# Optimization experiments

Hardware: AMD Instinct MI355X
Metric: run time of the kernel (lower is better)

## Reference

```python
import jax, jax.numpy as jnp
import numpy as np

IMG = 224
NUM_VIEWS = 6
K = 5  # splat kernel size (5x5 = 25 offsets)


def setup_inputs() -> dict:
    key = jax.random.key(0)
    points = jax.random.normal(key, (16, 32768, 3), dtype=jnp.float32)
    return {"points": points}


def _render(points):
    B, N, _ = points.shape
    deg2rad = jnp.pi / 180.0
    az = jnp.linspace(0.0, 360.0, NUM_VIEWS + 1)[:-1] * deg2rad          # (V,)
    el = jnp.array([0.0, 30.0, -30.0, 0.0, 0.0, 0.0])[:NUM_VIEWS] * deg2rad

    # 5x5 splat offsets in normalized coords, matching torch meshgrid(ij) + stack([dx,dy])
    off = jnp.linspace(-2.0 / IMG, 2.0 / IMG, K)
    dyg, dxg = jnp.meshgrid(off, off, indexing="ij")
    koff = jnp.stack([dxg, dyg], axis=-1).reshape(-1, 2)                  # (25, 2)

    def one_view(a, e):
        x, y, z = points[..., 0], points[..., 1], points[..., 2]
        x_rot = x * jnp.cos(a) - z * jnp.sin(a)
        z_rot = x * jnp.sin(a) + z * jnp.cos(a)
        y_rot = y * jnp.cos(e) - z_rot * jnp.sin(e)
        z_fin = y * jnp.sin(e) + z_rot * jnp.cos(e)                       # (B, N)
        p2d = jnp.stack([x_rot, y_rot], axis=-1)                          # (B, N, 2)

        zmin = jnp.min(z_fin, axis=1, keepdims=True)
        zmax = jnp.max(z_fin, axis=1, keepdims=True)
        feat = 0.3 + 0.7 * (z_fin - zmin) / (zmax - zmin + 1e-6)          # (B, N), in [0.3, 1.0]

        coords = p2d[:, :, None, :] + koff[None, None, :, :]              # (B, N, 25, 2)
        # torch .long() truncates toward zero; astype(int32) does too
        px = ((coords[..., 0] + 1.0) * 0.5 * (IMG - 1)).astype(jnp.int32)
        py = ((coords[..., 1] + 1.0) * 0.5 * (IMG - 1)).astype(jnp.int32)
        valid = (px >= 0) & (px < IMG) & (py >= 0) & (py < IMG)
        # invalid splats routed out-of-bounds and dropped by the scatter
        idx = jnp.where(valid, py * IMG + px, IMG * IMG).reshape(B, -1)   # (B, N*25)
        f = jnp.broadcast_to(feat[:, :, None], (B, N, K * K)).reshape(B, -1)

        def splat(i, fv):
            return jnp.zeros(IMG * IMG, dtype=points.dtype).at[i].max(fv, mode="drop")

        img = jax.vmap(splat)(idx, f).reshape(B, IMG, IMG)
        # all 3 channels receive the identical feature values
        return jnp.broadcast_to(img[:, None], (B, 3, IMG, IMG))

    views = jax.vmap(one_view)(az, el)                                    # (V, B, 3, H, W)
    return jnp.transpose(views, (1, 0, 2, 3, 4))                          # (B, V, 3, H, W)


def reference(points) -> jnp.ndarray:
    return _render(points)
```

## Files before the change

### kernel.cpp

```cpp
#include <hip/hip_runtime.h>
#include <math.h>

#define IMG    224
#define NVIEWS 6
#define BATCH  16
#define NPTS   32768
#define PLANE  (IMG * IMG)
#define HROWS  112
#define TILE_ELEMS (HROWS * IMG)

#define K1_NT    256
#define K1_CHUNK 8
#define K1_NWG   (BATCH * NVIEWS * K1_CHUNK)
#define SEGCAP   1024
#define NSEG     (K1_CHUNK * 4)

#define K2_NT    1024
#define K2_NWG   (BATCH * NVIEWS * 2)

#define WS_MM_OFF   24576
#define WS_BIN_OFF  65536

typedef float fx4 __attribute__((ext_vector_type(4)));

struct ViewTrig {
    float sa[NVIEWS], ca[NVIEWS], se[NVIEWS], ce[NVIEWS];
    float off0, off4;
};

__device__ __forceinline__ float fmul_(float a, float b) {
#pragma clang fp contract(off)
    return a * b;
}
__device__ __forceinline__ float fadd_(float a, float b) {
#pragma clang fp contract(off)
    return a + b;
}
__device__ __forceinline__ float fsub_(float a, float b) {
#pragma clang fp contract(off)
    return a - b;
}
__device__ __forceinline__ int pix_(float c) {
    return (int)fmul_(fadd_(c, 1.0f), 111.5f);
}

__device__ __forceinline__ unsigned fmap_(float f) {
    unsigned b = __float_as_uint(f);
    return b ^ ((unsigned)((int)b >> 31) | 0x80000000u);
}
__device__ __forceinline__ float fmap_inv_(unsigned u) {
    unsigned b = (u & 0x80000000u) ? (u ^ 0x80000000u) : ~u;
    return __uint_as_float(b);
}

__device__ __forceinline__ int lane_prefix_(unsigned long long m) {
    return __builtin_amdgcn_mbcnt_hi((unsigned)(m >> 32),
           __builtin_amdgcn_mbcnt_lo((unsigned)m, 0));
}

__global__ __launch_bounds__(K1_NT, 3) void transform_kernel(
    const float* __restrict__ pts, unsigned* __restrict__ ws, ViewTrig vt)
{
    const int bid   = blockIdx.x;
    const int chunk = bid & (K1_CHUNK - 1);
    const int v     = (bid >> 3) % NVIEWS;
    const int b     = bid / (K1_CHUNK * NVIEWS);
    const int bv    = b * NVIEWS + v;

    const float sa = vt.sa[v], ca = vt.ca[v], se = vt.se[v], ce = vt.ce[v];
    const float off0 = vt.off0, off4 = vt.off4;
    const float4* p4 = (const float4*)(pts + (size_t)b * NPTS * 3);

    const int tid = threadIdx.x, lane = tid & 63, wave = tid >> 6;
    const int segi = chunk * 4 + wave;

    unsigned* counts = ws;
    uint2* minmax = (uint2*)((char*)ws + WS_MM_OFF);
    uint2* bins   = (uint2*)((char*)ws + WS_BIN_OFF);
    uint2* seg0 = bins + ((size_t)((bv * 2 + 0) * NSEG + segi)) * SEGCAP;
    uint2* seg1 = bins + ((size_t)((bv * 2 + 1) * NSEG + segi)) * SEGCAP;

    unsigned q0 = 0, q1 = 0;
    float zmin = INFINITY, zmax = -INFINITY;

    auto do_point = [&](float x, float y, float z) {
        const float zr = fadd_(fmul_(x, sa), fmul_(z, ca));
        const float yr = fsub_(fmul_(y, ce), fmul_(zr, se));
        const float xr = fsub_(fmul_(x, ca), fmul_(z, sa));

        const int x0i = pix_(fadd_(xr, off0));
        const int x1i = pix_(fadd_(xr, off4));
        const int y0i = pix_(fadd_(yr, off0));
        const int y1i = pix_(fadd_(yr, off4));

        const float zf = fmaf(zr, ce, y * se);
        zmin = fminf(zmin, zf);
        zmax = fmaxf(zmax, zf);

        const bool okx = (x1i >= 0) && (x0i <= IMG - 1);
        const bool ok0 = okx && (y1i >= 0)     && (y0i <= HROWS - 1);
        const bool ok1 = okx && (y1i >= HROWS) && (y0i <= IMG - 1);

        const int cx0 = max(x0i, 0);
        const int cx1 = min(x1i, IMG - 1);
        const int cy0 = max(y0i, 0);
        const int cy1 = min(y1i, IMG - 1);
        const unsigned pk = (unsigned)cx0 | ((unsigned)cx1 << 8) |
                            ((unsigned)cy0 << 16) | ((unsigned)cy1 << 24);
        const unsigned fz = fmap_(zf);

        {
            const unsigned long long m = __ballot(ok0);
            if (ok0) seg0[q0 + lane_prefix_(m)] = make_uint2(fz, pk);
            q0 += (unsigned)__popcll(m);
        }
        {
            const unsigned long long m = __ballot(ok1);
            if (ok1) seg1[q1 + lane_prefix_(m)] = make_uint2(fz, pk);
            q1 += (unsigned)__popcll(m);
        }
    };

    #pragma unroll
    for (int kk = 0; kk < 4; ++kk) {
        const int g = chunk * 1024 + kk * K1_NT + tid;
        const float4 A = p4[3 * g + 0];
        const float4 B = p4[3 * g + 1];
        const float4 C = p4[3 * g + 2];
        do_point(A.x, A.y, A.z);
        do_point(A.w, B.x, B.y);
        do_point(B.z, B.w, C.x);
        do_point(C.y, C.z, C.w);
    }

    for (int o = 32; o > 0; o >>= 1) {
        zmin = fminf(zmin, __shfl_down(zmin, o, 64));
        zmax = fmaxf(zmax, __shfl_down(zmax, o, 64));
    }
    if (lane == 0) {
        counts[(bv * 2 + 0) * NSEG + segi] = q0;
        counts[(bv * 2 + 1) * NSEG + segi] = q1;
        minmax[bv * NSEG + segi] = make_uint2(fmap_(zmax), fmap_(-zmin));
    }
}

__global__ __launch_bounds__(K2_NT, 1) void splat_kernel(
    const unsigned* __restrict__ ws, float* __restrict__ out)
{
    extern __shared__ __align__(16) unsigned tile[];
    __shared__ unsigned pref[NSEG + 1];
    __shared__ float sScale, sBias;

    const int bid  = blockIdx.x;
    const int xcd  = bid & 7;
    const int slot = bid >> 3;
    const int hi   = (slot >= 12) ? 1 : 0;
    const int b    = xcd + 8 * hi;
    const int vh   = slot - 12 * hi;
    const int v    = vh >> 1;
    const int h    = vh & 1;
    const int bv   = b * NVIEWS + v;
    const int bvh  = bv * 2 + h;
    const int row0 = h * HROWS;
    const int row1 = row0 + HROWS - 1;

    const int tid = threadIdx.x, lane = tid & 63, wave = tid >> 6;

    const unsigned* counts = ws;
    const uint2* minmax = (const uint2*)((const char*)ws + WS_MM_OFF);
    const uint2* binb   = (const uint2*)((const char*)ws + WS_BIN_OFF)
                        + (size_t)bvh * NSEG * SEGCAP;

    {
        int4* t4 = (int4*)tile;
        for (int i = tid; i < TILE_ELEMS / 4; i += K2_NT)
            t4[i] = make_int4(0, 0, 0, 0);
    }
    if (wave == 0) {
        unsigned c = (lane < NSEG) ? counts[bvh * NSEG + lane] : 0u;
        unsigned inc = c;
        #pragma unroll
        for (int o = 1; o < NSEG; o <<= 1) {
            unsigned t = __shfl_up(inc, o, 64);
            if (lane >= o) inc += t;
        }
        if (lane < NSEG) pref[lane + 1] = inc;
        if (lane == 0)   pref[0] = 0;

        uint2 mm = (lane < NSEG) ? minmax[bv * NSEG + lane] : make_uint2(0u, 0u);
        for (int o = 32; o > 0; o >>= 1) {
            mm.x = max(mm.x, __shfl_down(mm.x, o, 64));
            mm.y = max(mm.y, __shfl_down(mm.y, o, 64));
        }
        if (lane == 0) {
            const float mx = fmap_inv_(mm.x);
            const float mn = -fmap_inv_(mm.y);
            const float scale = 0.7f / ((mx - mn) + 1e-6f);
            sScale = scale;
            sBias  = 0.3f - mn * scale;
        }
    }
    __syncthreads();

    const unsigned n = pref[NSEG];
    for (unsigned e = tid; e < n; e += K2_NT) {
        int s = 0;
        #pragma unroll
        for (int st = 16; st >= 1; st >>= 1)
            if (pref[s + st] <= e) s += st;
        const uint2 ent = binb[(size_t)s * SEGCAP + (e - pref[s])];
        const unsigned fz = ent.x, pk = ent.y;
        const int cx0 = pk & 255;
        const int cx1 = (pk >> 8) & 255;
        const int r0 = max((int)((pk >> 16) & 255), row0) - row0;
        const int r1 = min((int)(pk >> 24), row1) - row0;
        #pragma unroll
        for (int dy = 0; dy < 3; ++dy) {
            const int ry = r0 + dy;
            const bool yok = (ry <= r1);
            #pragma unroll
            for (int dx = 0; dx < 3; ++dx) {
                const int cx = cx0 + dx;
                if (yok && (cx <= cx1)) atomicMax(&tile[ry * IMG + cx], fz);
            }
        }
    }
    __syncthreads();

    const float scale = sScale, bias = sBias;

    float* dst = out + ((size_t)bv * 3) * PLANE + (size_t)row0 * IMG;
    const uint4* src = (const uint4*)tile;
    for (int i = tid; i < TILE_ELEMS / 4; i += K2_NT) {
        const uint4 u = src[i];
        fx4 f;
        f.x = (u.x == 0u) ? 0.0f : fmaf(fmap_inv_(u.x), scale, bias);
        f.y = (u.y == 0u) ? 0.0f : fmaf(fmap_inv_(u.y), scale, bias);
        f.z = (u.z == 0u) ? 0.0f : fmaf(fmap_inv_(u.z), scale, bias);
        f.w = (u.w == 0u) ? 0.0f : fmaf(fmap_inv_(u.w), scale, bias);
        #pragma unroll
        for (int c = 0; c < 3; ++c)
            __builtin_nontemporal_store(f, (fx4*)(dst + (size_t)c * PLANE) + i);
    }
}

extern "C" void kernel_launch(void* const* d_in, const int* in_sizes, int n_in,
                              void* d_out, int out_size, void* d_ws, size_t ws_size,
                              hipStream_t stream)
{
    const float* pts = (const float*)d_in[0];
    float* out = (float*)d_out;
    unsigned* ws = (unsigned*)d_ws;

    ViewTrig vt;
    const float d2r = (float)(M_PI / 180.0);
    const float el_deg[NVIEWS] = {0.0f, 30.0f, -30.0f, 0.0f, 0.0f, 0.0f};
    for (int v = 0; v < NVIEWS; ++v) {
        float a = (float)(60 * v) * d2r;
        float e = el_deg[v] * d2r;
        vt.sa[v] = (float)sin((double)a);
        vt.ca[v] = (float)cos((double)a);
        vt.se[v] = (float)sin((double)e);
        vt.ce[v] = (float)cos((double)e);
    }
    {
        const float s = (float)(2.0 / 224.0);
        vt.off0 = -s;
        vt.off4 = s;
    }

    (void)hipFuncSetAttribute(reinterpret_cast<const void*>(splat_kernel),
                              hipFuncAttributeMaxDynamicSharedMemorySize,
                              TILE_ELEMS * (int)sizeof(int));

    transform_kernel<<<K1_NWG, K1_NT, 0, stream>>>(pts, ws, vt);
    splat_kernel<<<K2_NWG, K2_NT, TILE_ELEMS * sizeof(int), stream>>>(ws, out);
}
```

Before: 93.78 us.

## Split splat into 4 row-band bins and 28-row tiles per workgroup

The transform kernel now sorts points into four 56-row bands instead of two halves. The splat kernel uses 768 workgroups of 512 threads, each covering a 28-row tile. Each workgroup scans the entries of its 56-row band and skips those that do not touch its 28 rows. The goal is more parallelism and occupancy from smaller LDS tiles, paid for by extra ballot/store work in the transform kernel and each band's entries being read twice.

```diff
diff --git a/kernel.cpp b/kernel.cpp
--- a/kernel.cpp
+++ b/kernel.cpp
@@ -6,20 +6,21 @@
 #define BATCH  16
 #define NPTS   32768
 #define PLANE  (IMG * IMG)
-#define HROWS  112
-#define TILE_ELEMS (HROWS * IMG)
 
 #define K1_NT    256
 #define K1_CHUNK 8
 #define K1_NWG   (BATCH * NVIEWS * K1_CHUNK)
 #define SEGCAP   1024
 #define NSEG     (K1_CHUNK * 4)
-
-#define K2_NT    1024
-#define K2_NWG   (BATCH * NVIEWS * 2)
-
-#define WS_MM_OFF   24576
-#define WS_BIN_OFF  65536
+#define NQUAD    4
+
+#define K2_NT    512
+#define OROWS    28
+#define OTILE    (OROWS * IMG)
+#define K2_NWG   (BATCH * NVIEWS * 8)
+
+#define WS_MM_OFF   49152
+#define WS_BIN_OFF  73728
 
 typedef float fx4 __attribute__((ext_vector_type(4)));
 
@@ -77,10 +78,12 @@
     unsigned* counts = ws;
     uint2* minmax = (uint2*)((char*)ws + WS_MM_OFF);
     uint2* bins   = (uint2*)((char*)ws + WS_BIN_OFF);
-    uint2* seg0 = bins + ((size_t)((bv * 2 + 0) * NSEG + segi)) * SEGCAP;
-    uint2* seg1 = bins + ((size_t)((bv * 2 + 1) * NSEG + segi)) * SEGCAP;
-
-    unsigned q0 = 0, q1 = 0;
+    uint2* seg[NQUAD];
+    #pragma unroll
+    for (int q = 0; q < NQUAD; ++q)
+        seg[q] = bins + ((size_t)((bv * NQUAD + q) * NSEG + segi)) * SEGCAP;
+
+    unsigned qn[NQUAD] = {0u, 0u, 0u, 0u};
     float zmin = INFINITY, zmax = -INFINITY;
 
     auto do_point = [&](float x, float y, float z) {
@@ -98,8 +101,6 @@
         zmax = fmaxf(zmax, zf);
 
         const bool okx = (x1i >= 0) && (x0i <= IMG - 1);
-        const bool ok0 = okx && (y1i >= 0)     && (y0i <= HROWS - 1);
-        const bool ok1 = okx && (y1i >= HROWS) && (y0i <= IMG - 1);
 
         const int cx0 = max(x0i, 0);
         const int cx1 = min(x1i, IMG - 1);
@@ -109,15 +110,12 @@
                             ((unsigned)cy0 << 16) | ((unsigned)cy1 << 24);
         const unsigned fz = fmap_(zf);
 
-        {
-            const unsigned long long m = __ballot(ok0);
-            if (ok0) seg0[q0 + lane_prefix_(m)] = make_uint2(fz, pk);
-            q0 += (unsigned)__popcll(m);
-        }
-        {
-            const unsigned long long m = __ballot(ok1);
-            if (ok1) seg1[q1 + lane_prefix_(m)] = make_uint2(fz, pk);
-            q1 += (unsigned)__popcll(m);
+        #pragma unroll
+        for (int q = 0; q < NQUAD; ++q) {
+            const bool ok = okx && (y1i >= 56 * q) && (y0i <= 56 * q + 55);
+            const unsigned long long m = __ballot(ok);
+            if (ok) seg[q][qn[q] + lane_prefix_(m)] = make_uint2(fz, pk);
+            qn[q] += (unsigned)__popcll(m);
         }
     };
 
@@ -138,13 +136,14 @@
         zmax = fmaxf(zmax, __shfl_down(zmax, o, 64));
     }
     if (lane == 0) {
-        counts[(bv * 2 + 0) * NSEG + segi] = q0;
-        counts[(bv * 2 + 1) * NSEG + segi] = q1;
+        #pragma unroll
+        for (int q = 0; q < NQUAD; ++q)
+            counts[(bv * NQUAD + q) * NSEG + segi] = qn[q];
         minmax[bv * NSEG + segi] = make_uint2(fmap_(zmax), fmap_(-zmin));
     }
 }
 
-__global__ __launch_bounds__(K2_NT, 1) void splat_kernel(
+__global__ __launch_bounds__(K2_NT, 6) void splat_kernel(
     const unsigned* __restrict__ ws, float* __restrict__ out)
 {
     extern __shared__ __align__(16) unsigned tile[];
@@ -154,30 +153,32 @@
     const int bid  = blockIdx.x;
     const int xcd  = bid & 7;
     const int slot = bid >> 3;
-    const int hi   = (slot >= 12) ? 1 : 0;
+    const int oct  = slot & 1;
+    const int rest = slot >> 1;
+    const int hi   = (rest >= 24) ? 1 : 0;
+    const int sub  = rest - 24 * hi;
+    const int v    = sub >> 2;
+    const int quad = sub & 3;
     const int b    = xcd + 8 * hi;
-    const int vh   = slot - 12 * hi;
-    const int v    = vh >> 1;
-    const int h    = vh & 1;
     const int bv   = b * NVIEWS + v;
-    const int bvh  = bv * 2 + h;
-    const int row0 = h * HROWS;
-    const int row1 = row0 + HROWS - 1;
+    const int bin  = bv * NQUAD + quad;
+    const int row0g = quad * 56 + oct * OROWS;
+    const int row1g = row0g + OROWS - 1;
 
     const int tid = threadIdx.x, lane = tid & 63, wave = tid >> 6;
 
     const unsigned* counts = ws;
     const uint2* minmax = (const uint2*)((const char*)ws + WS_MM_OFF);
     const uint2* binb   = (const uint2*)((const char*)ws + WS_BIN_OFF)
-                        + (size_t)bvh * NSEG * SEGCAP;
+                        + (size_t)bin * NSEG * SEGCAP;
 
     {
         int4* t4 = (int4*)tile;
-        for (int i = tid; i < TILE_ELEMS / 4; i += K2_NT)
+        for (int i = tid; i < OTILE / 4; i += K2_NT)
             t4[i] = make_int4(0, 0, 0, 0);
     }
     if (wave == 0) {
-        unsigned c = (lane < NSEG) ? counts[bvh * NSEG + lane] : 0u;
+        unsigned c = (lane < NSEG) ? counts[bin * NSEG + lane] : 0u;
         unsigned inc = c;
         #pragma unroll
         for (int o = 1; o < NSEG; o <<= 1) {
@@ -210,14 +211,16 @@
             if (pref[s + st] <= e) s += st;
         const uint2 ent = binb[(size_t)s * SEGCAP + (e - pref[s])];
         const unsigned fz = ent.x, pk = ent.y;
+        const int r0 = max((int)((pk >> 16) & 255), row0g);
+        const int r1 = min((int)(pk >> 24), row1g);
+        if (r0 > r1) continue;
         const int cx0 = pk & 255;
         const int cx1 = (pk >> 8) & 255;
-        const int r0 = max((int)((pk >> 16) & 255), row0) - row0;
-        const int r1 = min((int)(pk >> 24), row1) - row0;
+        const int rl = r0 - row0g, rh = r1 - row0g;
         #pragma unroll
         for (int dy = 0; dy < 3; ++dy) {
-            const int ry = r0 + dy;
-            const bool yok = (ry <= r1);
+            const int ry = rl + dy;
+            const bool yok = (ry <= rh);
             #pragma unroll
             for (int dx = 0; dx < 3; ++dx) {
                 const int cx = cx0 + dx;
@@ -229,9 +232,9 @@
 
     const float scale = sScale, bias = sBias;
 
-    float* dst = out + ((size_t)bv * 3) * PLANE + (size_t)row0 * IMG;
+    float* dst = out + ((size_t)bv * 3) * PLANE + (size_t)row0g * IMG;
     const uint4* src = (const uint4*)tile;
-    for (int i = tid; i < TILE_ELEMS / 4; i += K2_NT) {
+    for (int i = tid; i < OTILE / 4; i += K2_NT) {
         const uint4 u = src[i];
         fx4 f;
         f.x = (u.x == 0u) ? 0.0f : fmaf(fmap_inv_(u.x), scale, bias);
@@ -269,10 +272,6 @@
         vt.off4 = s;
     }
 
-    (void)hipFuncSetAttribute(reinterpret_cast<const void*>(splat_kernel),
-                              hipFuncAttributeMaxDynamicSharedMemorySize,
-                              TILE_ELEMS * (int)sizeof(int));
-
     transform_kernel<<<K1_NWG, K1_NT, 0, stream>>>(pts, ws, vt);
-    splat_kernel<<<K2_NWG, K2_NT, TILE_ELEMS * sizeof(int), stream>>>(ws, out);
-}
+    splat_kernel<<<K2_NWG, K2_NT, OTILE * sizeof(unsigned), stream>>>(ws, out);
+}
```

Result: no change. 92.51 us (-1.4%).
